# Kernel tuning notes

Measured on AMD Instinct MI355X. Metric: run time of the kernel, lower is better.

## Reference

```python
import jax, jax.numpy as jnp
import numpy as np

DROPOUT_P = 0.5  # pre-softmax dropout prob from __init__
_MASK_KEY = jax.random.key(42)  # fixed key -> deterministic dropout mask


def setup_inputs() -> dict:
    key = jax.random.key(0)
    kq, kk, kv = jax.random.split(key, 3)
    shape = (4, 16, 1024, 64)  # [B, H, S, D]
    Q = jax.random.normal(kq, shape, dtype=jnp.float32)
    K = jax.random.normal(kk, shape, dtype=jnp.float32)
    V = jax.random.normal(kv, shape, dtype=jnp.float32)
    return {"Q": Q, "K": K, "V": V}


def reference(Q, K, V):
    # scores: [B, H, S, S] = Q @ K^T  (no 1/sqrt(d) scaling: scale=False)
    scores = jnp.einsum("bhqd,bhkd->bhqk", Q, K)
    # pre-softmax dropout (train mode, p=0.5), deterministic fixed-key mask
    keep = jax.random.bernoulli(_MASK_KEY, 1.0 - DROPOUT_P, scores.shape)
    scores = jnp.where(keep, scores / (1.0 - DROPOUT_P), 0.0)
    attn = jax.nn.softmax(scores, axis=-1)
    return jnp.einsum("bhqk,bhkd->bhqd", attn, V)
```

## Files before the change

kernel.cpp:

```cpp
#include <hip/hip_runtime.h>
#include <hip/hip_bf16.h>
#include <hip/hip_fp16.h>

typedef _Float16 f16x8 __attribute__((ext_vector_type(8)));
typedef __fp16  h16x2 __attribute__((ext_vector_type(2)));
typedef float f32x4 __attribute__((ext_vector_type(4)));

#define S_LEN 1024
#define DH 64
#define KVB 64
#define NIT 16
#define KROW 72
#define PROW 40

__device__ __forceinline__ unsigned rotl(unsigned x, unsigned r) {
  return __builtin_amdgcn_alignbit(x, x, 32u - r);
}

__device__ __forceinline__ bool keep_bit(unsigned e) {
  const unsigned ks1 = 42u;
  const unsigned ks2 = 0x1BD11BF0u;
  unsigned x0 = 0u;
  unsigned x1 = e + ks1;
#define TFR(Ra,Rb,Rc,Rd) \
  x0 += x1; x1 = rotl(x1, Ra); x1 ^= x0; \
  x0 += x1; x1 = rotl(x1, Rb); x1 ^= x0; \
  x0 += x1; x1 = rotl(x1, Rc); x1 ^= x0; \
  x0 += x1; x1 = rotl(x1, Rd); x1 ^= x0;
  TFR(13u,15u,26u, 6u)  x0 += ks1; x1 += ks2 + 1u;
  TFR(17u,29u,16u,24u)  x0 += ks2; x1 += 2u;
  TFR(13u,15u,26u, 6u)     x1 += ks1 + 3u;
  TFR(17u,29u,16u,24u)  x0 += ks1; x1 += ks2 + 4u;
  TFR(13u,15u,26u, 6u)  x0 += ks2; x1 += 5u;
#undef TFR
  return ((x0 ^ x1) >> 31) == 0u;
}

__device__ __forceinline__ f16x8 pk8(f32x4 a, f32x4 b) {
  h16x2 p0 = __builtin_amdgcn_cvt_pkrtz(a[0], a[1]);
  h16x2 p1 = __builtin_amdgcn_cvt_pkrtz(a[2], a[3]);
  h16x2 p2 = __builtin_amdgcn_cvt_pkrtz(b[0], b[1]);
  h16x2 p3 = __builtin_amdgcn_cvt_pkrtz(b[2], b[3]);
  f16x8 r;
  r[0]=(_Float16)p0[0]; r[1]=(_Float16)p0[1]; r[2]=(_Float16)p1[0]; r[3]=(_Float16)p1[1];
  r[4]=(_Float16)p2[0]; r[5]=(_Float16)p2[1]; r[6]=(_Float16)p3[0]; r[7]=(_Float16)p3[1];
  return r;
}

__global__ __launch_bounds__(512)
void attn_dropout_kernel(const float* __restrict__ Q, const float* __restrict__ K,
                         const float* __restrict__ V, float* __restrict__ out) {
  __shared__ __align__(16) char smem[64*KROW*2*2 + 8*16*PROW*2];
  _Float16* Kl = (_Float16*)smem;
  _Float16* Vt = Kl + 64*KROW;
  _Float16* Pl = Vt + 64*KROW;

  const unsigned bh   = blockIdx.x >> 4;
  const unsigned q0   = (blockIdx.x & 15u) * 64u;
  const unsigned tid  = threadIdx.x;
  const unsigned w    = tid >> 6;
  const unsigned lane = tid & 63u;
  const unsigned g    = lane >> 4;
  const unsigned ln   = lane & 15u;
  const unsigned qw   = q0 + (w & 3u) * 16u;
  const unsigned koff = (w >> 2) * 32u;

  f16x8 Qa0, Qa1;
  {
    const float* Qp = Q + (size_t)(bh * S_LEN + qw + ln) * DH + g * 8;
    Qa0 = pk8(*(const f32x4*)(Qp),      *(const f32x4*)(Qp + 4));
    Qa1 = pk8(*(const f32x4*)(Qp + 32), *(const f32x4*)(Qp + 36));
  }

  float mrun[4], lrun[4];
  f32x4 accO[4];
#pragma unroll
  for (int r = 0; r < 4; ++r) { mrun[r] = -1e30f; lrun[r] = 0.0f; }
#pragma unroll
  for (int n = 0; n < 4; ++n) accO[n] = (f32x4){0.f, 0.f, 0.f, 0.f};

  const unsigned kk = tid >> 3;
  const unsigned dg = (tid & 7u) * 8u;

  for (int t = 0; t < NIT; ++t) {
    __syncthreads();
    {
      const float* Kp = K + (size_t)(bh * S_LEN + t * KVB + kk) * DH + dg;
      *(f16x8*)&Kl[kk * KROW + dg] = pk8(*(const f32x4*)Kp, *(const f32x4*)(Kp + 4));
    }
    {
      const float* Vp = V + (size_t)(bh * S_LEN + t * KVB + kk) * DH + dg;
      f32x4 v0 = *(const f32x4*)Vp;
      f32x4 v1 = *(const f32x4*)(Vp + 4);
#pragma unroll
      for (int i = 0; i < 4; ++i) {
        Vt[(dg + i) * KROW + kk]     = (_Float16)v0[i];
        Vt[(dg + 4 + i) * KROW + kk] = (_Float16)v1[i];
      }
    }
    __syncthreads();

    f32x4 sc[2];
#pragma unroll
    for (int nt = 0; nt < 2; ++nt) {
      const unsigned krow = koff + nt * 16 + ln;
      f16x8 kb0 = *(const f16x8*)&Kl[krow * KROW + g * 8];
      f16x8 kb1 = *(const f16x8*)&Kl[krow * KROW + 32 + g * 8];
      f32x4 a = (f32x4){0.f, 0.f, 0.f, 0.f};
      a = __builtin_amdgcn_mfma_f32_16x16x32_f16(Qa0, kb0, a, 0, 0, 0);
      a = __builtin_amdgcn_mfma_f32_16x16x32_f16(Qa1, kb1, a, 0, 0, 0);
      sc[nt] = a;
    }

    float sm[2][4];
#pragma unroll
    for (int nt = 0; nt < 2; ++nt) {
#pragma unroll
      for (int r = 0; r < 4; ++r) {
        unsigned q  = qw + g * 4 + r;
        unsigned kg = (unsigned)t * KVB + koff + nt * 16 + ln;
        unsigned e  = (bh << 20) + (q << 10) + kg;
        float s2 = sc[nt][r] * 2.0f;
        sm[nt][r] = keep_bit(e) ? s2 : 0.0f;
      }
    }

    float ps[2][4];
#pragma unroll
    for (int r = 0; r < 4; ++r) {
      float mx = fmaxf(sm[0][r], sm[1][r]);
#pragma unroll
      for (int off = 1; off < 16; off <<= 1) mx = fmaxf(mx, __shfl_xor(mx, off));
      float mn  = fmaxf(mrun[r], mx);
      float scl = __expf(mrun[r] - mn);
      mrun[r] = mn;
      float rs = 0.f;
#pragma unroll
      for (int nt = 0; nt < 2; ++nt) {
        float p = __expf(sm[nt][r] - mn);
        ps[nt][r] = p; rs += p;
      }
#pragma unroll
      for (int off = 1; off < 16; off <<= 1) rs += __shfl_xor(rs, off);
      lrun[r] = lrun[r] * scl + rs;
#pragma unroll
      for (int n = 0; n < 4; ++n) accO[n][r] *= scl;
    }

#pragma unroll
    for (int nt = 0; nt < 2; ++nt)
#pragma unroll
      for (int r = 0; r < 4; ++r)
        Pl[(w * 16 + g * 4 + r) * PROW + nt * 16 + ln] = (_Float16)ps[nt][r];

    f16x8 Pa = *(const f16x8*)&Pl[(w * 16 + ln) * PROW + g * 8];
#pragma unroll
    for (int nd = 0; nd < 4; ++nd) {
      f16x8 vb = *(const f16x8*)&Vt[(nd * 16 + ln) * KROW + koff + g * 8];
      accO[nd] = __builtin_amdgcn_mfma_f32_16x16x32_f16(Pa, vb, accO[nd], 0, 0, 0);
    }
  }

  float* Om = (float*)smem;
  float* Ml = Om + 64 * 68;
  __syncthreads();
  if (w >= 4) {
    const unsigned pq = (w & 3u) * 16u;
#pragma unroll
    for (int nd = 0; nd < 4; ++nd)
#pragma unroll
      for (int r = 0; r < 4; ++r)
        Om[(pq + g * 4 + r) * 68 + nd * 16 + ln] = accO[nd][r];
    if (ln == 0) {
#pragma unroll
      for (int r = 0; r < 4; ++r) {
        Ml[(pq + g * 4 + r) * 2 + 0] = mrun[r];
        Ml[(pq + g * 4 + r) * 2 + 1] = lrun[r];
      }
    }
  }
  __syncthreads();
  if (w < 4) {
    float e1[4], e2[4], lf[4];
#pragma unroll
    for (int r = 0; r < 4; ++r) {
      const unsigned pq = w * 16 + g * 4 + r;
      float m2 = Ml[pq * 2 + 0];
      float l2 = Ml[pq * 2 + 1];
      float m  = fmaxf(mrun[r], m2);
      e1[r] = __expf(mrun[r] - m);
      e2[r] = __expf(m2 - m);
      lf[r] = lrun[r] * e1[r] + l2 * e2[r];
    }
#pragma unroll
    for (int nd = 0; nd < 4; ++nd)
#pragma unroll
      for (int r = 0; r < 4; ++r) {
        const unsigned pq = w * 16 + g * 4 + r;
        float o = accO[nd][r] * e1[r] + Om[pq * 68 + nd * 16 + ln] * e2[r];
        out[(size_t)(bh * S_LEN + q0 + pq) * DH + nd * 16 + ln] = o / lf[r];
      }
  }
}

extern "C" void kernel_launch(void* const* d_in, const int* in_sizes, int n_in,
                              void* d_out, int out_size, void* d_ws, size_t ws_size,
                              hipStream_t stream) {
  const float* Q = (const float*)d_in[0];
  const float* K = (const float*)d_in[1];
  const float* V = (const float*)d_in[2];
  float* out = (float*)d_out;
  dim3 grid(64 * 16);
  dim3 block(512);
  hipLaunchKernelGGL(attn_dropout_kernel, grid, block, 0, stream, Q, K, V, out);
}
```

Before: 288.0 us.

## Fold dropout scale into log2 Q, lazy rescale softmax, prefetch next K/V tile

Pre-scales Q by 2/ln2 so scores come out directly in the log2 domain, and uses exp2f in place of expf with a separate multiply by 2. Skips the online-softmax max reduction and rescale unless some row's max grows past a threshold. Keeps the row sum per lane and reduces it once at the end. Also prefetches the next K/V tile into registers before the compute, and adds an occupancy hint to launch bounds. The lazy rescale risks fp16 overflow of P if the threshold is too loose, and the register prefetch raises register pressure.

```diff
diff --git a/kernel.cpp b/kernel.cpp
--- a/kernel.cpp
+++ b/kernel.cpp
@@ -1,6 +1,7 @@
 #include <hip/hip_runtime.h>
 #include <hip/hip_bf16.h>
 #include <hip/hip_fp16.h>
+#include <math.h>
 
 typedef _Float16 f16x8 __attribute__((ext_vector_type(8)));
 typedef __fp16  h16x2 __attribute__((ext_vector_type(2)));
@@ -12,6 +13,7 @@
 #define NIT 16
 #define KROW 72
 #define PROW 40
+#define THR 11.0f
 
 __device__ __forceinline__ unsigned rotl(unsigned x, unsigned r) {
   return __builtin_amdgcn_alignbit(x, x, 32u - r);
@@ -47,7 +49,7 @@
   return r;
 }
 
-__global__ __launch_bounds__(512)
+__global__ __launch_bounds__(512, 8)
 void attn_dropout_kernel(const float* __restrict__ Q, const float* __restrict__ K,
                          const float* __restrict__ V, float* __restrict__ out) {
   __shared__ __align__(16) char smem[64*KROW*2*2 + 8*16*PROW*2];
@@ -68,37 +70,50 @@
   f16x8 Qa0, Qa1;
   {
     const float* Qp = Q + (size_t)(bh * S_LEN + qw + ln) * DH + g * 8;
-    Qa0 = pk8(*(const f32x4*)(Qp),      *(const f32x4*)(Qp + 4));
-    Qa1 = pk8(*(const f32x4*)(Qp + 32), *(const f32x4*)(Qp + 36));
-  }
-
-  float mrun[4], lrun[4];
+    const float s = 2.885390082f;
+    f32x4 a = *(const f32x4*)(Qp)      * s;
+    f32x4 b = *(const f32x4*)(Qp + 4)  * s;
+    f32x4 c = *(const f32x4*)(Qp + 32) * s;
+    f32x4 d = *(const f32x4*)(Qp + 36) * s;
+    Qa0 = pk8(a, b);
+    Qa1 = pk8(c, d);
+  }
+
+  float mrun[4], lpart[4];
   f32x4 accO[4];
 #pragma unroll
-  for (int r = 0; r < 4; ++r) { mrun[r] = -1e30f; lrun[r] = 0.0f; }
+  for (int r = 0; r < 4; ++r) { mrun[r] = -1e30f; lpart[r] = 0.0f; }
 #pragma unroll
   for (int n = 0; n < 4; ++n) accO[n] = (f32x4){0.f, 0.f, 0.f, 0.f};
 
-  const unsigned kk = tid >> 3;
-  const unsigned dg = (tid & 7u) * 8u;
+  const unsigned kk  = tid >> 3;
+  const unsigned dgf = (tid & 7u) * 8u;
+
+  f32x4 kr0, kr1, vr0, vr1;
+  {
+    const float* Kp = K + (size_t)(bh * S_LEN + kk) * DH + dgf;
+    kr0 = *(const f32x4*)(Kp); kr1 = *(const f32x4*)(Kp + 4);
+    const float* Vp = V + (size_t)(bh * S_LEN + kk) * DH + dgf;
+    vr0 = *(const f32x4*)(Vp); vr1 = *(const f32x4*)(Vp + 4);
+  }
 
   for (int t = 0; t < NIT; ++t) {
     __syncthreads();
+    *(f16x8*)&Kl[kk * KROW + dgf] = pk8(kr0, kr1);
+#pragma unroll
+    for (int i = 0; i < 4; ++i) {
+      Vt[(dgf + i) * KROW + kk]     = (_Float16)vr0[i];
+      Vt[(dgf + 4 + i) * KROW + kk] = (_Float16)vr1[i];
+    }
+    __syncthreads();
+
     {
-      const float* Kp = K + (size_t)(bh * S_LEN + t * KVB + kk) * DH + dg;
-      *(f16x8*)&Kl[kk * KROW + dg] = pk8(*(const f32x4*)Kp, *(const f32x4*)(Kp + 4));
-    }
-    {
-      const float* Vp = V + (size_t)(bh * S_LEN + t * KVB + kk) * DH + dg;
-      f32x4 v0 = *(const f32x4*)Vp;
-      f32x4 v1 = *(const f32x4*)(Vp + 4);
-#pragma unroll
-      for (int i = 0; i < 4; ++i) {
-        Vt[(dg + i) * KROW + kk]     = (_Float16)v0[i];
-        Vt[(dg + 4 + i) * KROW + kk] = (_Float16)v1[i];
-      }
-    }
-    __syncthreads();
+      int tn = (t + 1 < NIT) ? t + 1 : NIT - 1;
+      const float* Kp = K + (size_t)(bh * S_LEN + tn * KVB + kk) * DH + dgf;
+      kr0 = *(const f32x4*)(Kp); kr1 = *(const f32x4*)(Kp + 4);
+      const float* Vp = V + (size_t)(bh * S_LEN + tn * KVB + kk) * DH + dgf;
+      vr0 = *(const f32x4*)(Vp); vr1 = *(const f32x4*)(Vp + 4);
+    }
 
     f32x4 sc[2];
 #pragma unroll
@@ -112,7 +127,8 @@
       sc[nt] = a;
     }
 
-    float sm[2][4];
+    float s[2][4];
+    float pmx[4];
 #pragma unroll
     for (int nt = 0; nt < 2; ++nt) {
 #pragma unroll
@@ -120,38 +136,38 @@
         unsigned q  = qw + g * 4 + r;
         unsigned kg = (unsigned)t * KVB + koff + nt * 16 + ln;
         unsigned e  = (bh << 20) + (q << 10) + kg;
-        float s2 = sc[nt][r] * 2.0f;
-        sm[nt][r] = keep_bit(e) ? s2 : 0.0f;
-      }
-    }
-
-    float ps[2][4];
-#pragma unroll
-    for (int r = 0; r < 4; ++r) {
-      float mx = fmaxf(sm[0][r], sm[1][r]);
-#pragma unroll
-      for (int off = 1; off < 16; off <<= 1) mx = fmaxf(mx, __shfl_xor(mx, off));
-      float mn  = fmaxf(mrun[r], mx);
-      float scl = __expf(mrun[r] - mn);
-      mrun[r] = mn;
-      float rs = 0.f;
-#pragma unroll
-      for (int nt = 0; nt < 2; ++nt) {
-        float p = __expf(sm[nt][r] - mn);
-        ps[nt][r] = p; rs += p;
-      }
-#pragma unroll
-      for (int off = 1; off < 16; off <<= 1) rs += __shfl_xor(rs, off);
-      lrun[r] = lrun[r] * scl + rs;
-#pragma unroll
-      for (int n = 0; n < 4; ++n) accO[n][r] *= scl;
-    }
-
-#pragma unroll
-    for (int nt = 0; nt < 2; ++nt)
-#pragma unroll
-      for (int r = 0; r < 4; ++r)
-        Pl[(w * 16 + g * 4 + r) * PROW + nt * 16 + ln] = (_Float16)ps[nt][r];
+        s[nt][r] = keep_bit(e) ? sc[nt][r] : 0.0f;
+      }
+    }
+#pragma unroll
+    for (int r = 0; r < 4; ++r) pmx[r] = fmaxf(s[0][r], s[1][r]);
+
+    bool need = (pmx[0] > mrun[0] + THR) | (pmx[1] > mrun[1] + THR) |
+                (pmx[2] > mrun[2] + THR) | (pmx[3] > mrun[3] + THR);
+    if (__any(need)) {
+#pragma unroll
+      for (int r = 0; r < 4; ++r) {
+        float mx = pmx[r];
+#pragma unroll
+        for (int off = 1; off < 16; off <<= 1) mx = fmaxf(mx, __shfl_xor(mx, off));
+        float mn  = fmaxf(mrun[r], mx);
+        float scl = exp2f(mrun[r] - mn);
+        mrun[r] = mn;
+        lpart[r] *= scl;
+#pragma unroll
+        for (int n = 0; n < 4; ++n) accO[n][r] *= scl;
+      }
+    }
+
+#pragma unroll
+    for (int nt = 0; nt < 2; ++nt) {
+#pragma unroll
+      for (int r = 0; r < 4; ++r) {
+        float p = exp2f(s[nt][r] - mrun[r]);
+        lpart[r] += p;
+        Pl[(w * 16 + g * 4 + r) * PROW + nt * 16 + ln] = (_Float16)p;
+      }
+    }
 
     f16x8 Pa = *(const f16x8*)&Pl[(w * 16 + ln) * PROW + g * 8];
 #pragma unroll
@@ -159,6 +175,14 @@
       f16x8 vb = *(const f16x8*)&Vt[(nd * 16 + ln) * KROW + koff + g * 8];
       accO[nd] = __builtin_amdgcn_mfma_f32_16x16x32_f16(Pa, vb, accO[nd], 0, 0, 0);
     }
+  }
+
+#pragma unroll
+  for (int r = 0; r < 4; ++r) {
+    float l = lpart[r];
+#pragma unroll
+    for (int off = 1; off < 16; off <<= 1) l += __shfl_xor(l, off);
+    lpart[r] = l;
   }
 
   float* Om = (float*)smem;
@@ -175,7 +199,7 @@
 #pragma unroll
       for (int r = 0; r < 4; ++r) {
         Ml[(pq + g * 4 + r) * 2 + 0] = mrun[r];
-        Ml[(pq + g * 4 + r) * 2 + 1] = lrun[r];
+        Ml[(pq + g * 4 + r) * 2 + 1] = lpart[r];
       }
     }
   }
@@ -188,9 +212,9 @@
       float m2 = Ml[pq * 2 + 0];
       float l2 = Ml[pq * 2 + 1];
       float m  = fmaxf(mrun[r], m2);
-      e1[r] = __expf(mrun[r] - m);
-      e2[r] = __expf(m2 - m);
-      lf[r] = lrun[r] * e1[r] + l2 * e2[r];
+      e1[r] = exp2f(mrun[r] - m);
+      e2[r] = exp2f(m2 - m);
+      lf[r] = lpart[r] * e1[r] + l2 * e2[r];
     }
 #pragma unroll
     for (int nd = 0; nd < 4; ++nd)
```

Result: slower. 334.4 us (+16.1%).
